# Kernel optimization log

Measured on AMD Instinct MI355X. Metric: run time of the kernel, lower is better.

Reference implementation:

```python
import jax, jax.numpy as jnp
import numpy as np

B, S, D, H = 2, 2048, 1024, 16
DK = D // H


def setup_inputs() -> dict:
    key = jax.random.key(0)
    ks = jax.random.split(key, 9)
    w_scale = 1.0 / np.sqrt(D)  # xavier-ish scale
    return {
        "q": jax.random.normal(ks[0], (B, S, D), dtype=jnp.float32),
        "k": jax.random.normal(ks[1], (B, S, D), dtype=jnp.float32),
        "v": jax.random.normal(ks[2], (B, S, D), dtype=jnp.float32),
        "A": jax.random.uniform(ks[3], (S, S), dtype=jnp.float32),
        "Wq": jax.random.normal(ks[4], (D, D), dtype=jnp.float32) * w_scale,
        "bq": jnp.zeros((D,), jnp.float32),
        "Wk": jax.random.normal(ks[5], (D, D), dtype=jnp.float32) * w_scale,
        "bk": jnp.zeros((D,), jnp.float32),
        "Wv": jax.random.normal(ks[6], (D, D), dtype=jnp.float32) * w_scale,
        "bv": jnp.zeros((D,), jnp.float32),
        "Wo": jax.random.normal(ks[7], (D, D), dtype=jnp.float32) * w_scale,
        "bo": jnp.zeros((D,), jnp.float32),
    }


def _proj(x, W, b):
    # nn.Linear: x @ W^T + b, then split heads -> [B, H, S, DK]
    y = jnp.einsum("bsd,ed->bse", x, W) + b
    return y.reshape(B, S, H, DK).transpose(0, 2, 1, 3)


def reference(q, k, v, A, Wq, bq, Wk, bk, Wv, bv, Wo, bo):
    qh = _proj(q, Wq, bq)  # [B,H,S,DK]
    kh = _proj(k, Wk, bk)
    vh = _proj(v, Wv, bv)
    scale = 1.0 / jnp.sqrt(jnp.asarray(DK, qh.dtype))
    scores = jnp.einsum("bhqd,bhkd->bhqk", qh, kh) * scale  # [B,H,S,S]
    # No softmax: scores multiplied by structural mask A^T (dropout disabled, eval)
    p_attn = scores * A.T
    x = jnp.einsum("bhqk,bhkd->bhqd", p_attn, vh)
    x = x.transpose(0, 2, 1, 3).reshape(B, S, D)
    return jnp.einsum("bsd,ed->bse", x, Wo) + bo
```

## Files before the change

### kernel.cpp

```cpp
#include <hip/hip_runtime.h>

#define SEQ    2048
#define DMODEL 1024
#define NHEAD  16
#define DHEAD  64
#define NBATCH 2

typedef __bf16 bf16x8 __attribute__((ext_vector_type(8)));
typedef float f32x16 __attribute__((ext_vector_type(16)));
typedef float f32x8 __attribute__((ext_vector_type(8)));
typedef unsigned short ushort8v __attribute__((ext_vector_type(8)));
typedef unsigned int uint2v __attribute__((ext_vector_type(2)));
typedef int int4v __attribute__((ext_vector_type(4)));

static __device__ __forceinline__ unsigned short f2b(float f){
  unsigned int u = __builtin_bit_cast(unsigned int, f);
  u += 0x7fffu + ((u>>16)&1u);
  return (unsigned short)(u>>16);
}
static __device__ __forceinline__ float b2f(unsigned short h){
  unsigned int u = ((unsigned int)h)<<16;
  return __builtin_bit_cast(float, u);
}
static __device__ __forceinline__ f32x16 mfma32(bf16x8 a, bf16x8 b, f32x16 c){
  return __builtin_amdgcn_mfma_f32_32x32x16_bf16(a,b,c,0,0,0);
}
static __device__ __forceinline__ ushort8v cvt8(const float* p){
  float4 f0 = *(const float4*)p;
  float4 f1 = *(const float4*)(p+4);
  ushort8v r;
  r[0]=f2b(f0.x); r[1]=f2b(f0.y); r[2]=f2b(f0.z); r[3]=f2b(f0.w);
  r[4]=f2b(f1.x); r[5]=f2b(f1.y); r[6]=f2b(f1.z); r[7]=f2b(f1.w);
  return r;
}
#define GLOAD16(g,l) __builtin_amdgcn_global_load_lds( \
    (const __attribute__((address_space(1))) void*)(g), \
    (__attribute__((address_space(3))) void*)(l), 16, 0, 0)

__global__ __launch_bounds__(256) void cvtXpack(
    const float* __restrict__ q, const float* __restrict__ k, const float* __restrict__ v,
    unsigned short* __restrict__ Xq, unsigned short* __restrict__ Xk, unsigned short* __restrict__ Xv)
{
  const int z = blockIdx.z;
  const float* S = (z==0)? q : (z==1)? k : v;
  unsigned short* D = (z==0)? Xq : (z==1)? Xk : Xv;
  const int g = blockIdx.x;
  const int wave = threadIdx.x>>6, lane = threadIdx.x&63;
  const int l31 = lane&31, hi = lane>>5;
  const float* src = S + (size_t)(g*32 + l31)*DMODEL + 8*hi + 256*wave;
  unsigned short* dst = D + (size_t)(g*64 + wave*16)*512 + lane*8;
  #pragma unroll
  for (int i=0;i<16;i++)
    *(ushort8v*)(dst + (size_t)i*512) = cvt8(src + 16*i);
}

__global__ __launch_bounds__(256) void cvtWpack(
    const float* __restrict__ Wq, const float* __restrict__ Wk,
    const float* __restrict__ Wv, const float* __restrict__ Wo,
    unsigned short* __restrict__ Wp)
{
  const int z = blockIdx.z;
  const float* S = (z==0)? Wq : (z==1)? Wk : (z==2)? Wv : Wo;
  const int g = blockIdx.x;
  const int wave = threadIdx.x>>6, lane = threadIdx.x&63;
  const int l31 = lane&31, hi = lane>>5;
  const float* src = S + (size_t)(g*32 + l31)*DMODEL + 8*hi + 256*wave;
  unsigned short* dst = Wp + (size_t)((z*32 + g)*64 + wave*16)*512 + lane*8;
  #pragma unroll
  for (int i=0;i<16;i++)
    *(ushort8v*)(dst + (size_t)i*512) = cvt8(src + 16*i);
}

__global__ __launch_bounds__(256) void cvtA(const float* __restrict__ A,
                                            unsigned short* __restrict__ Am){
  const int tid  = threadIdx.x;
  const int lane = tid&63, l31 = lane&31, hi = lane>>5;
  const int q32  = blockIdx.x;
  const int kt   = blockIdx.y*4 + (tid>>6);
  const int q    = q32*32 + l31;

  unsigned short out8[4][8];
  #pragma unroll
  for (int fi=0; fi<2; fi++){
    #pragma unroll
    for (int mm=0; mm<4; mm++){
      #pragma unroll
      for (int j=0; j<4; j++){
        const int k = kt*64 + 32*fi + 8*mm + 4*hi + j;
        out8[fi*2 + (mm>>1)][(mm&1)*4 + j] = f2b(A[(size_t)k*SEQ + q]);
      }
    }
  }
  unsigned short* dst = Am + ((size_t)(q32*32 + kt)*4)*512 + lane*8;
  #pragma unroll
  for (int w=0; w<4; w++)
    *(ushort8v*)(dst + (size_t)w*512) = *(const ushort8v*)out8[w];
}

__global__ __launch_bounds__(256,3) void proj_qkv(
    const unsigned short* __restrict__ Xq, const unsigned short* __restrict__ Xk, const unsigned short* __restrict__ Xv,
    const unsigned short* __restrict__ Wp,
    const float* __restrict__ bq, const float* __restrict__ bk, const float* __restrict__ bv,
    unsigned short* __restrict__ qh, unsigned short* __restrict__ Kp, unsigned short* __restrict__ Vp)
{
  const int z = blockIdx.z;
  const unsigned short* X = (z==0)? Xq : (z==1)? Xk : Xv;
  const unsigned short* W = Wp + (size_t)z*1048576;
  const float* bias = (z==0)? bq : (z==1)? bk : bv;
  const float alpha = (z==0)? 0.125f : 1.0f;

  const int orig = blockIdx.y*8 + blockIdx.x;
  const int virt = (orig&7)*32 + (orig>>3);
  const int bx = virt&7, by = virt>>3;
  const int mb = by*128, nb = bx*128;

  const int tid = threadIdx.x;
  const int lane = tid&63, wave = tid>>6;
  const int wr = wave>>1, wc = wave&1, l31 = lane&31, hi = lane>>5;
  f32x16 acc[2][2] = {};

  const unsigned short* a0p = X + (size_t)((mb>>5) + 2*wr)*32768 + lane*8;
  const unsigned short* a1p = a0p + 32768;
  const unsigned short* b0p = W + (size_t)((nb>>5) + 2*wc)*32768 + lane*8;
  const unsigned short* b1p = b0p + 32768;

  #pragma unroll 4
  for (int s=0;s<64;s++){
    bf16x8 a0 = *(const bf16x8*)(a0p + (size_t)s*512);
    bf16x8 a1 = *(const bf16x8*)(a1p + (size_t)s*512);
    bf16x8 b0 = *(const bf16x8*)(b0p + (size_t)s*512);
    bf16x8 b1 = *(const bf16x8*)(b1p + (size_t)s*512);
    acc[0][0] = mfma32(a0,b0,acc[0][0]);
    acc[0][1] = mfma32(a0,b1,acc[0][1]);
    acc[1][0] = mfma32(a1,b0,acc[1][0]);
    acc[1][1] = mfma32(a1,b1,acc[1][1]);
  }

  #pragma unroll
  for (int fj=0; fj<2; fj++){
    const int e = nb + 64*wc + 32*fj + l31;
    const float bv_ = bias[e];
    const int hh = e>>6, dk = e&63;
    #pragma unroll
    for (int fi=0; fi<2; fi++){
      #pragma unroll
      for (int r=0;r<16;r++){
        const int i = mb + 64*wr + 32*fi + (r&3) + 8*(r>>2) + 4*hi;
        const int bb = i>>11, ss = i&(SEQ-1);
        const int bhh = bb*NHEAD + hh;
        const unsigned short val = f2b((acc[fi][fj][r] + bv_)*alpha);
        if (z==0){
          qh[((size_t)bhh*SEQ + ss)*DHEAD + dk] = val;
        } else if (z==1){
          const size_t addr = (((size_t)(bhh*64 + (ss>>5))*4 + (dk>>4))*64
                               + ((dk>>3)&1)*32 + (ss&31))*8 + (dk&7);
          Kp[addr] = val;
        } else {
          const size_t addr = ((((size_t)(bhh*32 + (ss>>6))*4 + ((ss>>4)&3))*2
                               + (dk>>5))*64 + ((ss>>3)&1)*32 + (dk&31))*8 + (ss&7);
          Vp[addr] = val;
        }
      }
    }
  }
}

__global__ __launch_bounds__(256,2) void attn(
    const unsigned short* __restrict__ qh, const unsigned short* __restrict__ Kp,
    const unsigned short* __restrict__ Vp, const unsigned short* __restrict__ Am,
    unsigned short* __restrict__ xp)
{
  const int orig = blockIdx.y*16 + blockIdx.x;
  const int xcd = orig&7, within = orig>>3;
  const int bh   = xcd*4 + (within>>4);
  const int qblk = within&15;

  const int tid  = threadIdx.x;
  const int lane = tid&63, wave = tid>>6;
  const int l31 = lane&31, hi = lane>>5;

  const int q32  = qblk*4 + wave;
  const int qrow = q32*32 + l31;
  const unsigned short* qp = qh + ((size_t)bh*SEQ + qrow)*DHEAD;
  bf16x8 Qf[4];
  #pragma unroll
  for (int t=0;t<4;t++) Qf[t] = *(const bf16x8*)(qp + 16*t + 8*hi);

  f32x16 xacc[2] = {};

  const unsigned short* kpb = Kp + (size_t)bh*131072 + lane*8;
  const unsigned short* vpb = Vp + (size_t)bh*131072 + lane*8;
  const unsigned short* apb = Am + (size_t)q32*65536 + lane*8;

  __shared__ unsigned short Klds[2][4096];
  __shared__ unsigned short Vlds[2][4096];

  ushort8v Aa[4], Ab[4];

  #define STAGE(BUF, KT) { \
    const unsigned short* _k = kpb + (size_t)(KT)*4096; \
    const unsigned short* _v = vpb + (size_t)(KT)*4096; \
    GLOAD16(_k + (size_t)(2*wave  )*512, &Klds[BUF][(2*wave  )*512]); \
    GLOAD16(_k + (size_t)(2*wave+1)*512, &Klds[BUF][(2*wave+1)*512]); \
    GLOAD16(_v + (size_t)(2*wave  )*512, &Vlds[BUF][(2*wave  )*512]); \
    GLOAD16(_v + (size_t)(2*wave+1)*512, &Vlds[BUF][(2*wave+1)*512]); }

  #define LOADA(DST, KT) { \
    const unsigned short* _ap = apb + (size_t)(KT)*2048; \
    _Pragma("unroll") \
    for (int w=0;w<4;w++) DST[w] = *(const ushort8v*)(_ap + (size_t)w*512); }

  STAGE(0, 0);
  LOADA(Aa, 0);
  __syncthreads();

  #define BODY(KT, BUF, AR, AN) { \
    STAGE((BUF)^1, ((KT)+1)&31); \
    LOADA(AN, ((KT)+1)&31); \
    unsigned int wv[2][4], xv[2][4]; \
    _Pragma("unroll") \
    for (int fi=0; fi<2; fi++){ \
      f32x16 sacc = {}; \
      _Pragma("unroll") \
      for (int s=0;s<4;s++){ \
        bf16x8 kf = *(const bf16x8*)&Klds[BUF][(fi*4+s)*512 + lane*8]; \
        sacc = mfma32(kf, Qf[s], sacc); \
      } \
      ushort8v a80 = AR[fi*2+0], a81 = AR[fi*2+1]; \
      _Pragma("unroll") \
      for (int mm=0; mm<4; mm++){ \
        const int b0 = (mm&1)*4, rb2 = 4*mm; \
        float p0 = sacc[rb2+0]*((mm>>1)? b2f(a81[b0+0]) : b2f(a80[b0+0])); \
        float p1 = sacc[rb2+1]*((mm>>1)? b2f(a81[b0+1]) : b2f(a80[b0+1])); \
        float p2 = sacc[rb2+2]*((mm>>1)? b2f(a81[b0+2]) : b2f(a80[b0+2])); \
        float p3 = sacc[rb2+3]*((mm>>1)? b2f(a81[b0+3]) : b2f(a80[b0+3])); \
        asm("v_cvt_pk_bf16_f32 %0, %1, %2" : "=v"(wv[fi][mm]) : "v"(p0), "v"(p1)); \
        asm("v_cvt_pk_bf16_f32 %0, %1, %2" : "=v"(xv[fi][mm]) : "v"(p2), "v"(p3)); \
      } \
    } \
    __builtin_amdgcn_s_setprio(1); \
    _Pragma("unroll") \
    for (int s2=0; s2<4; s2++){ \
      const int fi = s2>>1, sl = s2&1; \
      uint2v rw = __builtin_amdgcn_permlane32_swap(wv[fi][2*sl], wv[fi][2*sl+1], false, false); \
      uint2v rx = __builtin_amdgcn_permlane32_swap(xv[fi][2*sl], xv[fi][2*sl+1], false, false); \
      int4v av; av.x = (int)rw[0]; av.y = (int)rx[0]; av.z = (int)rw[1]; av.w = (int)rx[1]; \
      bf16x8 pa = __builtin_bit_cast(bf16x8, av); \
      bf16x8 v0 = *(const bf16x8*)&Vlds[BUF][(s2*2+0)*512 + lane*8]; \
      bf16x8 v1 = *(const bf16x8*)&Vlds[BUF][(s2*2+1)*512 + lane*8]; \
      xacc[0] = mfma32(pa, v0, xacc[0]); \
      xacc[1] = mfma32(pa, v1, xacc[1]); \
    } \
    __builtin_amdgcn_s_setprio(0); \
    __syncthreads(); }

  #pragma unroll 1
  for (int tt=0; tt<16; tt++){
    BODY(2*tt,   0, Aa, Ab);
    BODY(2*tt+1, 1, Ab, Aa);
  }
  #undef BODY
  #undef STAGE
  #undef LOADA

  const int b = bh>>4, h = bh&15;
  #pragma unroll
  for (int fj=0; fj<2; fj++){
    const int scol = h*4 + fj*2 + (l31>>4);
    const int lpart = ((l31>>3)&1)*32;
    const int epart = l31&7;
    #pragma unroll
    for (int r=0;r<16;r++){
      const int qq = q32*32 + (r&3) + 8*(r>>2) + 4*hi;
      const int row = b*SEQ + qq;
      const size_t addr = ((size_t)(row>>5)*64 + scol)*512 + (lpart + (row&31))*8 + epart;
      xp[addr] = f2b(xacc[fj][r]);
    }
  }
}

__global__ __launch_bounds__(256,4) void oproj(
    const unsigned short* __restrict__ Xp, const unsigned short* __restrict__ Wop,
    const float* __restrict__ bo, float* __restrict__ out)
{
  const int orig = blockIdx.y*16 + blockIdx.x;
  const int virt = (orig&7)*64 + (orig>>3);
  const int bx = virt&15, by = virt>>4;
  const int mb = by*128, nb = bx*64;

  const int tid = threadIdx.x;
  const int lane = tid&63, wave = tid>>6;
  const int l31 = lane&31, hi = lane>>5;
  f32x16 acc[2] = {};

  const unsigned short* ap  = Xp  + (size_t)((mb>>5) + wave)*32768 + lane*8;
  const unsigned short* b0p = Wop + (size_t)(nb>>5)*32768 + lane*8;
  const unsigned short* b1p = b0p + 32768;

  #pragma unroll 4
  for (int s=0;s<64;s++){
    bf16x8 a  = *(const bf16x8*)(ap  + (size_t)s*512);
    bf16x8 b0 = *(const bf16x8*)(b0p + (size_t)s*512);
    bf16x8 b1 = *(const bf16x8*)(b1p + (size_t)s*512);
    acc[0] = mfma32(a,b0,acc[0]);
    acc[1] = mfma32(a,b1,acc[1]);
  }

  #pragma unroll
  for (int fj=0; fj<2; fj++){
    const int e = nb + 32*fj + l31;
    const float bv_ = bo[e];
    #pragma unroll
    for (int r=0;r<16;r++){
      const int i = mb + 32*wave + (r&3) + 8*(r>>2) + 4*hi;
      out[(size_t)i*DMODEL + e] = acc[fj][r] + bv_;
    }
  }
}

extern "C" void kernel_launch(void* const* d_in, const int* in_sizes, int n_in,
                              void* d_out, int out_size, void* d_ws, size_t ws_size,
                              hipStream_t stream)
{
  const float* q  = (const float*)d_in[0];
  const float* k  = (const float*)d_in[1];
  const float* v  = (const float*)d_in[2];
  const float* A  = (const float*)d_in[3];
  const float* Wq = (const float*)d_in[4];
  const float* bq = (const float*)d_in[5];
  const float* Wk = (const float*)d_in[6];
  const float* bk = (const float*)d_in[7];
  const float* Wv = (const float*)d_in[8];
  const float* bv = (const float*)d_in[9];
  const float* Wo = (const float*)d_in[10];
  const float* bo = (const float*)d_in[11];
  float* out = (float*)d_out;

  unsigned short* ws = (unsigned short*)d_ws;
  const size_t NE = (size_t)NBATCH*SEQ*DMODEL;
  unsigned short* qh  = ws;
  unsigned short* Kp  = qh + NE;
  unsigned short* Vp  = Kp + NE;
  unsigned short* xb  = Vp + NE;
  unsigned short* Wp  = xb + NE;
  unsigned short* Xqp = (unsigned short*)d_out;
  unsigned short* Xkp = Xqp + NE;
  unsigned short* Am  = (unsigned short*)d_out;
  unsigned short* Xvp = xb;

  cvtXpack<<<dim3(128, 1, 3), 256, 0, stream>>>(q, k, v, Xqp, Xkp, Xvp);
  cvtWpack<<<dim3(32, 1, 4), 256, 0, stream>>>(Wq, Wk, Wv, Wo, Wp);
  proj_qkv<<<dim3(8, 32, 3), 256, 0, stream>>>(
      Xqp, Xkp, Xvp, Wp, bq, bk, bv, qh, Kp, Vp);
  cvtA<<<dim3(64, 8), 256, 0, stream>>>(A, Am);
  attn<<<dim3(16, 32), 256, 0, stream>>>(qh, Kp, Vp, Am, xb);
  oproj<<<dim3(16, 32), 256, 0, stream>>>(xb, Wp + (size_t)3*1048576, bo, out);
}
```

Before: 133.7 us.

## Split attention key tiles across two wave groups with LDS reduction

```diff
diff --git a/kernel.cpp b/kernel.cpp
--- a/kernel.cpp
+++ b/kernel.cpp
@@ -165,7 +165,7 @@
   }
 }
 
-__global__ __launch_bounds__(256,2) void attn(
+__global__ __launch_bounds__(512,4) void attn(
     const unsigned short* __restrict__ qh, const unsigned short* __restrict__ Kp,
     const unsigned short* __restrict__ Vp, const unsigned short* __restrict__ Am,
     unsigned short* __restrict__ xp)
@@ -177,9 +177,10 @@
 
   const int tid  = threadIdx.x;
   const int lane = tid&63, wave = tid>>6;
+  const int qsub = wave&3, khalf = wave>>2;
   const int l31 = lane&31, hi = lane>>5;
 
-  const int q32  = qblk*4 + wave;
+  const int q32  = qblk*4 + qsub;
   const int qrow = q32*32 + l31;
   const unsigned short* qp = qh + ((size_t)bh*SEQ + qrow)*DHEAD;
   bf16x8 Qf[4];
@@ -192,23 +193,24 @@
   const unsigned short* vpb = Vp + (size_t)bh*131072 + lane*8;
   const unsigned short* apb = Am + (size_t)q32*65536 + lane*8;
 
-  __shared__ unsigned short Klds[2][4096];
-  __shared__ unsigned short Vlds[2][4096];
-
-  ushort8v Aa[4], Ab[4];
+  __shared__ float SMEMf[8448];
+  unsigned short* smem = (unsigned short*)SMEMf;
+
+  const unsigned short* gsb = ((wave<4)? kpb : vpb);
+  const int fo = (wave&3)*2;
+  const int dof = ((wave<4)? 0 : 4096) + fo*512;
+
+  ushort8v Aa[2], Ab[2];
 
   #define STAGE(BUF, KT) { \
-    const unsigned short* _k = kpb + (size_t)(KT)*4096; \
-    const unsigned short* _v = vpb + (size_t)(KT)*4096; \
-    GLOAD16(_k + (size_t)(2*wave  )*512, &Klds[BUF][(2*wave  )*512]); \
-    GLOAD16(_k + (size_t)(2*wave+1)*512, &Klds[BUF][(2*wave+1)*512]); \
-    GLOAD16(_v + (size_t)(2*wave  )*512, &Vlds[BUF][(2*wave  )*512]); \
-    GLOAD16(_v + (size_t)(2*wave+1)*512, &Vlds[BUF][(2*wave+1)*512]); }
+    const unsigned short* _g = gsb + (size_t)(KT)*4096 + (size_t)fo*512; \
+    GLOAD16(_g,       smem + (BUF)*8192 + dof); \
+    GLOAD16(_g + 512, smem + (BUF)*8192 + dof + 512); }
 
   #define LOADA(DST, KT) { \
-    const unsigned short* _ap = apb + (size_t)(KT)*2048; \
-    _Pragma("unroll") \
-    for (int w=0;w<4;w++) DST[w] = *(const ushort8v*)(_ap + (size_t)w*512); }
+    const unsigned short* _ap = apb + (size_t)(KT)*2048 + (size_t)(khalf*2)*512; \
+    DST[0] = *(const ushort8v*)(_ap); \
+    DST[1] = *(const ushort8v*)(_ap + 512); }
 
   STAGE(0, 0);
   LOADA(Aa, 0);
@@ -217,16 +219,15 @@
   #define BODY(KT, BUF, AR, AN) { \
     STAGE((BUF)^1, ((KT)+1)&31); \
     LOADA(AN, ((KT)+1)&31); \
-    unsigned int wv[2][4], xv[2][4]; \
-    _Pragma("unroll") \
-    for (int fi=0; fi<2; fi++){ \
+    unsigned int wv[4], xv[4]; \
+    { \
       f32x16 sacc = {}; \
       _Pragma("unroll") \
       for (int s=0;s<4;s++){ \
-        bf16x8 kf = *(const bf16x8*)&Klds[BUF][(fi*4+s)*512 + lane*8]; \
+        bf16x8 kf = *(const bf16x8*)(smem + (BUF)*8192 + (khalf*4+s)*512 + lane*8); \
         sacc = mfma32(kf, Qf[s], sacc); \
       } \
-      ushort8v a80 = AR[fi*2+0], a81 = AR[fi*2+1]; \
+      ushort8v a80 = AR[0], a81 = AR[1]; \
       _Pragma("unroll") \
       for (int mm=0; mm<4; mm++){ \
         const int b0 = (mm&1)*4, rb2 = 4*mm; \
@@ -234,20 +235,20 @@
         float p1 = sacc[rb2+1]*((mm>>1)? b2f(a81[b0+1]) : b2f(a80[b0+1])); \
         float p2 = sacc[rb2+2]*((mm>>1)? b2f(a81[b0+2]) : b2f(a80[b0+2])); \
         float p3 = sacc[rb2+3]*((mm>>1)? b2f(a81[b0+3]) : b2f(a80[b0+3])); \
-        asm("v_cvt_pk_bf16_f32 %0, %1, %2" : "=v"(wv[fi][mm]) : "v"(p0), "v"(p1)); \
-        asm("v_cvt_pk_bf16_f32 %0, %1, %2" : "=v"(xv[fi][mm]) : "v"(p2), "v"(p3)); \
+        asm("v_cvt_pk_bf16_f32 %0, %1, %2" : "=v"(wv[mm]) : "v"(p0), "v"(p1)); \
+        asm("v_cvt_pk_bf16_f32 %0, %1, %2" : "=v"(xv[mm]) : "v"(p2), "v"(p3)); \
       } \
     } \
     __builtin_amdgcn_s_setprio(1); \
     _Pragma("unroll") \
-    for (int s2=0; s2<4; s2++){ \
-      const int fi = s2>>1, sl = s2&1; \
-      uint2v rw = __builtin_amdgcn_permlane32_swap(wv[fi][2*sl], wv[fi][2*sl+1], false, false); \
-      uint2v rx = __builtin_amdgcn_permlane32_swap(xv[fi][2*sl], xv[fi][2*sl+1], false, false); \
+    for (int sl=0; sl<2; sl++){ \
+      const int s2 = 2*khalf + sl; \
+      uint2v rw = __builtin_amdgcn_permlane32_swap(wv[2*sl], wv[2*sl+1], false, false); \
+      uint2v rx = __builtin_amdgcn_permlane32_swap(xv[2*sl], xv[2*sl+1], false, false); \
       int4v av; av.x = (int)rw[0]; av.y = (int)rx[0]; av.z = (int)rw[1]; av.w = (int)rx[1]; \
       bf16x8 pa = __builtin_bit_cast(bf16x8, av); \
-      bf16x8 v0 = *(const bf16x8*)&Vlds[BUF][(s2*2+0)*512 + lane*8]; \
-      bf16x8 v1 = *(const bf16x8*)&Vlds[BUF][(s2*2+1)*512 + lane*8]; \
+      bf16x8 v0 = *(const bf16x8*)(smem + (BUF)*8192 + 4096 + (s2*2+0)*512 + lane*8); \
+      bf16x8 v1 = *(const bf16x8*)(smem + (BUF)*8192 + 4096 + (s2*2+1)*512 + lane*8); \
       xacc[0] = mfma32(pa, v0, xacc[0]); \
       xacc[1] = mfma32(pa, v1, xacc[1]); \
     } \
@@ -263,18 +264,34 @@
   #undef STAGE
   #undef LOADA
 
-  const int b = bh>>4, h = bh&15;
-  #pragma unroll
-  for (int fj=0; fj<2; fj++){
-    const int scol = h*4 + fj*2 + (l31>>4);
-    const int lpart = ((l31>>3)&1)*32;
-    const int epart = l31&7;
-    #pragma unroll
-    for (int r=0;r<16;r++){
-      const int qq = q32*32 + (r&3) + 8*(r>>2) + 4*hi;
-      const int row = b*SEQ + qq;
-      const size_t addr = ((size_t)(row>>5)*64 + scol)*512 + (lpart + (row&31))*8 + epart;
-      xp[addr] = f2b(xacc[fj][r]);
+  float* red = SMEMf;
+  if (khalf==1){
+    #pragma unroll
+    for (int j=0;j<2;j++)
+      #pragma unroll
+      for (int r=0;r<16;r++)
+        red[((qsub*64 + lane)*33) + 16*j + r] = xacc[j][r];
+  }
+  __syncthreads();
+  if (khalf==0){
+    #pragma unroll
+    for (int j=0;j<2;j++)
+      #pragma unroll
+      for (int r=0;r<16;r++)
+        xacc[j][r] += red[((qsub*64 + lane)*33) + 16*j + r];
+    const int b = bh>>4, h = bh&15;
+    #pragma unroll
+    for (int fj=0; fj<2; fj++){
+      const int scol = h*4 + fj*2 + (l31>>4);
+      const int lpart = ((l31>>3)&1)*32;
+      const int epart = l31&7;
+      #pragma unroll
+      for (int r=0;r<16;r++){
+        const int qq = q32*32 + (r&3) + 8*(r>>2) + 4*hi;
+        const int row = b*SEQ + qq;
+        const size_t addr = ((size_t)(row>>5)*64 + scol)*512 + (lpart + (row&31))*8 + epart;
+        xp[addr] = f2b(xacc[fj][r]);
+      }
     }
   }
 }
@@ -353,6 +370,6 @@
   proj_qkv<<<dim3(8, 32, 3), 256, 0, stream>>>(
       Xqp, Xkp, Xvp, Wp, bq, bk, bv, qh, Kp, Vp);
   cvtA<<<dim3(64, 8), 256, 0, stream>>>(A, Am);
-  attn<<<dim3(16, 32), 256, 0, stream>>>(qh, Kp, Vp, Am, xb);
+  attn<<<dim3(16, 32), 512, 0, stream>>>(qh, Kp, Vp, Am, xb);
   oproj<<<dim3(16, 32), 256, 0, stream>>>(xb, Wp + (size_t)3*1048576, bo, out);
 }
```

After: 133.5 us. No clear change (-0.2%).
